# Kernel tuning notes

Measured on AMD Instinct MI355X. Metric: run time of the kernel, lower is better.

Reference implementation:

```python
import jax, jax.numpy as jnp
import numpy as np

DIM = 4096
N_HEADS = 32
N_KV_HEADS = 8
HEAD_DIM = 128
WINDOW = 1024
SEQ = 2048
ROPE_THETA = 10000.0


def setup_inputs() -> dict:
    key = jax.random.key(0)
    ks = jax.random.split(key, 5)
    x = jax.random.normal(ks[0], (SEQ, DIM), dtype=jnp.float32)
    # torch nn.Linear weights are [out_features, in_features]
    wq = jax.random.normal(ks[1], (N_HEADS * HEAD_DIM, DIM), dtype=jnp.float32) * (DIM ** -0.5)
    wk = jax.random.normal(ks[2], (N_KV_HEADS * HEAD_DIM, DIM), dtype=jnp.float32) * (DIM ** -0.5)
    wv = jax.random.normal(ks[3], (N_KV_HEADS * HEAD_DIM, DIM), dtype=jnp.float32) * (DIM ** -0.5)
    wo = jax.random.normal(ks[4], (DIM, N_HEADS * HEAD_DIM), dtype=jnp.float32) * ((N_HEADS * HEAD_DIM) ** -0.5)
    # RoPE freqs: freqs_cis[t, i] = exp(1j * t * theta^(-2i/d)); store cos/sin
    inv_freq = ROPE_THETA ** (-jnp.arange(0, HEAD_DIM, 2, dtype=jnp.float32) / HEAD_DIM)  # [D/2]
    angles = jnp.arange(SEQ, dtype=jnp.float32)[:, None] * inv_freq[None, :]  # [S, D/2]
    return {"x": x, "wq": wq, "wk": wk, "wv": wv, "wo": wo,
            "cos": jnp.cos(angles), "sin": jnp.sin(angles)}


def _apply_rope(t, cos, sin):
    # t: [S, H, D]; cos/sin: [S, D/2] -> rotate consecutive pairs as complex mul
    S, H, D = t.shape
    tr = t.reshape(S, H, D // 2, 2)
    t0, t1 = tr[..., 0], tr[..., 1]
    c = cos[:, None, :]
    s = sin[:, None, :]
    out = jnp.stack([t0 * c - t1 * s, t0 * s + t1 * c], axis=-1)
    return out.reshape(S, H, D)


def reference(x, wq, wk, wv, wo, cos, sin):
    S = x.shape[0]
    repeats = N_HEADS // N_KV_HEADS
    scale = HEAD_DIM ** -0.5
    q = (x @ wq.T).reshape(S, N_HEADS, HEAD_DIM)
    k = (x @ wk.T).reshape(S, N_KV_HEADS, HEAD_DIM)
    v = (x @ wv.T).reshape(S, N_KV_HEADS, HEAD_DIM)
    q = _apply_rope(q, cos, sin)
    k = _apply_rope(k, cos, sin)
    # repeat_kv: repeat_interleave along head axis (GQA)
    k = jnp.repeat(k, repeats, axis=1)  # [S, H, D]
    v = jnp.repeat(v, repeats, axis=1)
    scores = jnp.einsum('qhd,khd->hqk', q, k) * scale  # [H, S, S]
    # sliding-window causal mask: attend to j in (i - WINDOW, i]
    i = jnp.arange(S)[:, None]
    j = jnp.arange(S)[None, :]
    allowed = (j <= i) & (i - j < WINDOW)  # [S, S]
    scores = jnp.where(allowed[None, :, :], scores, jnp.finfo(scores.dtype).min)
    probs = jax.nn.softmax(scores, axis=-1)
    out = jnp.einsum('hqk,khd->qhd', probs, v).reshape(S, N_HEADS * HEAD_DIM)
    return out @ wo.T
```

## Files before the change

kernel.cpp:

```cpp
#include <hip/hip_runtime.h>

#define DIM 4096
#define NH 32
#define NKV 8
#define HD 128
#define WINDOW 1024
#define SEQ 2048

typedef unsigned int uint32;
typedef __attribute__((ext_vector_type(8))) short short8_t;
typedef __attribute__((ext_vector_type(8))) __bf16 bf16x8_t;
typedef __attribute__((ext_vector_type(4))) float floatx4_t;

__device__ __forceinline__ uint32 f2bf_bits(float f) {
  uint32 u = __builtin_bit_cast(uint32, f);
  return (u + 0x7fffu + ((u >> 16) & 1u)) >> 16;
}
__device__ __forceinline__ float bf2f(unsigned short b) {
  return __builtin_bit_cast(float, ((uint32)b) << 16);
}

template <class X, class Y> struct same_t { static constexpr bool v = false; };
template <class X> struct same_t<X, X> { static constexpr bool v = true; };

__device__ __forceinline__ void load_lds16(const unsigned short* g, unsigned short* l) {
  __builtin_amdgcn_global_load_lds((__attribute__((address_space(1))) void*)g,
                                   (__attribute__((address_space(3))) void*)l, 16, 0, 0);
}

template <typename TC>
__global__ __launch_bounds__(256) void gemm_bf16(const unsigned short* __restrict__ A,
                                                 const unsigned short* __restrict__ B,
                                                 TC* __restrict__ C,
                                                 int M, int N, int K) {
  __shared__ unsigned short As[128 * 64];
  __shared__ unsigned short Bs[128 * 64];
  const int tid = threadIdx.x;
  const int lane = tid & 63, w = tid >> 6;
  const int quad = lane >> 4, l16 = lane & 15;
  const int wm = w >> 1, wn = w & 1;
  const size_t m0 = (size_t)blockIdx.y * 128, n0 = (size_t)blockIdx.x * 128;

  const int srow = tid >> 3;
  const int scol = ((tid & 7) ^ (srow & 7)) << 3;
  const unsigned short* Abase = A + (m0 + srow) * (size_t)K + scol;
  const unsigned short* Bbase = B + (n0 + srow) * (size_t)K + scol;
  unsigned short* ldsA = As + (tid >> 6) * 512;
  unsigned short* ldsB = Bs + (tid >> 6) * 512;

  const int sa = l16 & 7;
  const int raA = wm * 64 + l16;
  const int raB = wn * 64 + l16;

  floatx4_t acc[4][4] = {};

  const int nk = K >> 6;
  for (int kt = 0; kt < nk; kt++) {
    const int kbase = kt << 6;
#pragma unroll
    for (int i = 0; i < 4; i++) {
      load_lds16(Abase + kbase + (size_t)(i * 32) * K, ldsA + i * 2048);
      load_lds16(Bbase + kbase + (size_t)(i * 32) * K, ldsB + i * 2048);
    }
    __syncthreads();
#pragma unroll
    for (int ks = 0; ks < 2; ks++) {
      bf16x8_t af[4], bfg[4];
#pragma unroll
      for (int i = 0; i < 4; i++) {
        const int colA = (((ks << 2) | quad) ^ sa) << 3;
        af[i] = __builtin_bit_cast(bf16x8_t,
            *(const short8_t*)(&As[(raA + i * 16) * 64 + colA]));
      }
#pragma unroll
      for (int j = 0; j < 4; j++) {
        const int colB = (((ks << 2) | quad) ^ sa) << 3;
        bfg[j] = __builtin_bit_cast(bf16x8_t,
            *(const short8_t*)(&Bs[(raB + j * 16) * 64 + colB]));
      }
#pragma unroll
      for (int i = 0; i < 4; i++)
#pragma unroll
        for (int j = 0; j < 4; j++)
          acc[i][j] = __builtin_amdgcn_mfma_f32_16x16x32_bf16(af[i], bfg[j], acc[i][j], 0, 0, 0);
    }
    __syncthreads();
  }
#pragma unroll
  for (int i = 0; i < 4; i++)
#pragma unroll
    for (int j = 0; j < 4; j++)
#pragma unroll
      for (int r = 0; r < 4; r++) {
        size_t row = m0 + wm * 64 + i * 16 + quad * 4 + r;
        size_t col = n0 + wn * 64 + j * 16 + l16;
        float v = acc[i][j][r];
        if constexpr (same_t<TC, float>::v)
          C[row * (size_t)N + col] = v;
        else
          C[row * (size_t)N + col] = (unsigned short)f2bf_bits(v);
      }
}

__global__ __launch_bounds__(256) void cvt_kernel(const float* __restrict__ in,
                                                  unsigned short* __restrict__ out, int n8) {
  int idx = blockIdx.x * 256 + threadIdx.x;
  if (idx >= n8) return;
  const float4* p = (const float4*)in + (size_t)idx * 2;
  float4 a = p[0], b = p[1];
  uint32 w0 = f2bf_bits(a.x) | (f2bf_bits(a.y) << 16);
  uint32 w1 = f2bf_bits(a.z) | (f2bf_bits(a.w) << 16);
  uint32 w2 = f2bf_bits(b.x) | (f2bf_bits(b.y) << 16);
  uint32 w3 = f2bf_bits(b.z) | (f2bf_bits(b.w) << 16);
  ((uint4*)out)[idx] = make_uint4(w0, w1, w2, w3);
}

__global__ __launch_bounds__(256) void rope_kernel(unsigned short* __restrict__ t,
                                                   const float* __restrict__ cosp,
                                                   const float* __restrict__ sinp,
                                                   int H, int ld) {
  const int idx = blockIdx.x * 256 + threadIdx.x;
  const int j = idx & 63;
  const int rem = idx >> 6;
  const int hh = rem % H;
  const int s = rem / H;
  const size_t base = (size_t)s * ld + hh * 128 + (j << 1);
  const float t0 = bf2f(t[base]), t1 = bf2f(t[base + 1]);
  const float c = cosp[s * 64 + j], sn = sinp[s * 64 + j];
  t[base] = (unsigned short)f2bf_bits(t0 * c - t1 * sn);
  t[base + 1] = (unsigned short)f2bf_bits(t0 * sn + t1 * c);
}

__global__ __launch_bounds__(256) void vtrans_kernel(const unsigned short* __restrict__ v,
                                                     unsigned short* __restrict__ vT) {
  __shared__ unsigned short t[64][72];
  const int s0 = blockIdx.y * 64, r0 = blockIdx.x * 64;
  const int tid = threadIdx.x;
#pragma unroll
  for (int it = 0; it < 2; it++) {
    int f = it * 256 + tid;
    int si = f >> 3, cj = (f & 7) << 3;
    *(short8_t*)(&t[si][cj]) = *(const short8_t*)(v + (size_t)(s0 + si) * 2048 + r0 + cj);
  }
  __syncthreads();
#pragma unroll
  for (int it = 0; it < 2; it++) {
    int f = it * 256 + tid;
    int ri = f >> 3, sj = (f & 7) << 3;
    short8_t o;
#pragma unroll
    for (int jj = 0; jj < 8; jj++) o[jj] = t[sj + jj][ri];
    *(short8_t*)(vT + (size_t)(r0 + ri) * SEQ + s0 + sj) = o;
  }
}

__global__ __launch_bounds__(256, 3) void attn_kernel(const unsigned short* __restrict__ qb,
                                                      const unsigned short* __restrict__ kb,
                                                      const unsigned short* __restrict__ vT,
                                                      unsigned short* __restrict__ attn_out) {
  const int h = blockIdx.x;
  const int qt = 31 - blockIdx.y;
  const int kvh = h >> 2;
  const int q0 = qt * 64;
  const int tid = threadIdx.x;
  const int w = tid >> 6, lane = tid & 63;
  const int quad = lane >> 4, l16 = lane & 15;
  const float SCALE = 0.08838834764831845f;

  __shared__ unsigned short Ks[64 * 128];
  __shared__ unsigned short VTs[128 * 64];
  __shared__ unsigned short PTs[4 * 64 * 34];

  unsigned short* pt = &PTs[w * 2176];

  const int krow = tid >> 4;
  const int kc16 = tid & 15;
  const int kgcol = (kc16 ^ (krow & 7)) << 3;
  const unsigned short* kgbase = kb + (size_t)krow * 2048 + kvh * 128 + kgcol;
  const int vrow = tid >> 3;
  const int vc8 = tid & 7;
  const int vgcol = (vc8 ^ (vrow & 7)) << 3;
  const unsigned short* vgbase = vT + (size_t)(kvh * 128 + vrow) * 2048 + vgcol;
  unsigned short* ldsK = Ks + w * 512;
  unsigned short* ldsV = VTs + w * 512;

  bf16x8_t aq[4];
  {
    const unsigned short* qp = qb + (size_t)(q0 + w * 16 + l16) * 4096 + h * 128 + quad * 8;
#pragma unroll
    for (int ks = 0; ks < 4; ks++)
      aq[ks] = __builtin_bit_cast(bf16x8_t, *(const short8_t*)(qp + ks * 32));
  }

  floatx4_t O[8] = {};
  float m_run[4], l_run[4];
#pragma unroll
  for (int r = 0; r < 4; r++) { m_run[r] = -3e38f; l_run[r] = 0.0f; }

  const int qmin = q0 + w * 16, qmax = qmin + 15;
  int kbeg = q0 - (WINDOW - 1); if (kbeg < 0) kbeg = 0;
  const int c0 = kbeg & ~63;
  const int nch = (q0 + 64 - c0) >> 6;
  const int sa = l16 & 7;

  for (int ci = 0; ci < nch; ci++) {
    const int kb0 = c0 + (ci << 6);
#pragma unroll
    for (int i = 0; i < 4; i++)
      load_lds16(kgbase + (size_t)(kb0 + i * 16) * 2048, ldsK + i * 2048);
#pragma unroll
    for (int i = 0; i < 4; i++)
      load_lds16(vgbase + kb0 + (size_t)(i * 32) * 2048, ldsV + i * 2048);
    __syncthreads();
    floatx4_t S[4];
#pragma unroll
    for (int j = 0; j < 4; j++) {
      floatx4_t acc = {};
      const int keyrow = j * 16 + l16;
#pragma unroll
      for (int ks = 0; ks < 4; ks++) {
        const int c16 = ((ks << 2) | quad) ^ sa;
        bf16x8_t bfk = __builtin_bit_cast(bf16x8_t,
            *(const short8_t*)(&Ks[keyrow * 128 + c16 * 8]));
        acc = __builtin_amdgcn_mfma_f32_16x16x32_bf16(aq[ks], bfk, acc, 0, 0, 0);
      }
      S[j] = acc;
    }
    const bool need_mask = (kb0 + 63 > qmin) || (qmax - kb0 >= WINDOW);
    if (need_mask) {
#pragma unroll
      for (int j = 0; j < 4; j++) {
        const int key = kb0 + j * 16 + l16;
#pragma unroll
        for (int r = 0; r < 4; r++) {
          const int i = qmin + quad * 4 + r;
          const bool ok = (key <= i) && (i - key < WINDOW);
          S[j][r] = ok ? S[j][r] : -3e38f;
        }
      }
    }
    float mx[4], rs[4], alpha[4];
#pragma unroll
    for (int r = 0; r < 4; r++) {
      float m = S[0][r];
#pragma unroll
      for (int j = 1; j < 4; j++) m = fmaxf(m, S[j][r]);
#pragma unroll
      for (int d = 1; d < 16; d <<= 1) m = fmaxf(m, __shfl_xor(m, d, 16));
      mx[r] = fmaxf(m_run[r], m);
      alpha[r] = __expf(SCALE * (m_run[r] - mx[r]));
      m_run[r] = mx[r];
      rs[r] = 0.0f;
    }
#pragma unroll
    for (int j = 0; j < 4; j++) {
      float p[4];
#pragma unroll
      for (int r = 0; r < 4; r++) {
        const float sv = S[j][r];
        float e = __expf(SCALE * (sv - mx[r]));
        if (need_mask) e = (sv < -1e37f) ? 0.0f : e;
        p[r] = e;
        rs[r] += e;
      }
      uint32* dst = (uint32*)(pt + (j * 16 + l16) * 34 + quad * 4);
      dst[0] = f2bf_bits(p[0]) | (f2bf_bits(p[1]) << 16);
      dst[1] = f2bf_bits(p[2]) | (f2bf_bits(p[3]) << 16);
    }
#pragma unroll
    for (int r = 0; r < 4; r++) {
#pragma unroll
      for (int d = 1; d < 16; d <<= 1) rs[r] += __shfl_xor(rs[r], d, 16);
      l_run[r] = l_run[r] * alpha[r] + rs[r];
    }
#pragma unroll
    for (int nt = 0; nt < 8; nt++)
#pragma unroll
      for (int r = 0; r < 4; r++) O[nt][r] *= alpha[r];
    asm volatile("" ::: "memory");
#pragma unroll
    for (int ks = 0; ks < 2; ks++) {
      short8_t as;
#pragma unroll
      for (int jj = 0; jj < 8; jj++)
        as[jj] = (short)pt[(ks * 32 + quad * 8 + jj) * 34 + l16];
      bf16x8_t af = __builtin_bit_cast(bf16x8_t, as);
#pragma unroll
      for (int nt = 0; nt < 8; nt++) {
        const int c8 = (((ks << 2) | quad) ^ sa);
        bf16x8_t bfv = __builtin_bit_cast(bf16x8_t,
            *(const short8_t*)(&VTs[(nt * 16 + l16) * 64 + c8 * 8]));
        O[nt] = __builtin_amdgcn_mfma_f32_16x16x32_bf16(af, bfv, O[nt], 0, 0, 0);
      }
    }
    __syncthreads();
  }
  float inv_l[4];
#pragma unroll
  for (int r = 0; r < 4; r++) inv_l[r] = 1.0f / l_run[r];
#pragma unroll
  for (int nt = 0; nt < 8; nt++)
#pragma unroll
    for (int r = 0; r < 4; r++) {
      float v = O[nt][r] * inv_l[r];
      attn_out[(size_t)(qmin + quad * 4 + r) * 4096 + h * 128 + nt * 16 + l16] =
          (unsigned short)f2bf_bits(v);
    }
}

extern "C" void kernel_launch(void* const* d_in, const int* in_sizes, int n_in,
                              void* d_out, int out_size, void* d_ws, size_t ws_size,
                              hipStream_t stream) {
  (void)in_sizes; (void)n_in; (void)out_size; (void)ws_size;
  const float* x    = (const float*)d_in[0];
  const float* wq   = (const float*)d_in[1];
  const float* wk   = (const float*)d_in[2];
  const float* wv   = (const float*)d_in[3];
  const float* wo   = (const float*)d_in[4];
  const float* cosp = (const float*)d_in[5];
  const float* sinp = (const float*)d_in[6];
  float* out = (float*)d_out;
  char* ws = (char*)d_ws;

  unsigned short* wqb   = (unsigned short*)(ws);
  unsigned short* attnb = (unsigned short*)(ws);
  unsigned short* vTb   = (unsigned short*)(ws + 16777216);
  unsigned short* xb    = (unsigned short*)(ws + 33554432);
  unsigned short* wkvb  = (unsigned short*)(ws + 33554432 + 16777216);
  unsigned short* wob   = (unsigned short*)(ws + 33554432);
  unsigned short* qb    = (unsigned short*)(ws + 67108864);
  unsigned short* kvb   = (unsigned short*)(ws + 83886080);

  cvt_kernel<<<4096, 256, 0, stream>>>(x, xb, SEQ * DIM / 8);
  cvt_kernel<<<8192, 256, 0, stream>>>(wq, wqb, NH * HD * DIM / 8);
  cvt_kernel<<<2048, 256, 0, stream>>>(wk, wkvb, NKV * HD * DIM / 8);
  cvt_kernel<<<2048, 256, 0, stream>>>(wv, wkvb + (size_t)NKV * HD * DIM, NKV * HD * DIM / 8);
  gemm_bf16<unsigned short><<<dim3(32, 16), 256, 0, stream>>>(xb, wqb, qb, SEQ, 4096, DIM);
  gemm_bf16<unsigned short><<<dim3(16, 16), 256, 0, stream>>>(xb, wkvb, kvb, SEQ, 2048, DIM);
  cvt_kernel<<<8192, 256, 0, stream>>>(wo, wob, DIM * NH * HD / 8);
  rope_kernel<<<SEQ * NH * 64 / 256, 256, 0, stream>>>(qb, cosp, sinp, NH, 4096);
  rope_kernel<<<SEQ * NKV * 64 / 256, 256, 0, stream>>>(kvb, cosp, sinp, NKV, 2048);
  vtrans_kernel<<<dim3(16, 32), 256, 0, stream>>>(kvb + 1024, vTb);
  attn_kernel<<<dim3(NH, 32), 256, 0, stream>>>(qb, kvb, vTb, attnb);
  gemm_bf16<float><<<dim3(32, 16), 256, 0, stream>>>(attnb, wob, out, SEQ, 4096, DIM);
}
```

Before: 530.0 us.

## Fuse QKV projection into one GEMM with RoPE epilogue and batched conversion

Concatenates the Q, K and V weights into one bf16 matrix and computes the three projections with a single GEMM of width 6144. RoPE is applied in the GEMM epilogue using a lane shuffle to fetch each pair partner, which removes both separate rope kernels and their read-modify-write passes. The four fp32-to-bf16 conversions for x, wq, wk and wv are merged into one launch, and the workspace layout and attention strides are updated for the new 6144-wide qkv buffer. The costs are cos/sin loads in the GEMM epilogue and a different workspace aliasing scheme that must stay correct.

```diff
diff --git a/kernel.cpp b/kernel.cpp
--- a/kernel.cpp
+++ b/kernel.cpp
@@ -6,6 +6,7 @@
 #define HD 128
 #define WINDOW 1024
 #define SEQ 2048
+#define QLD 6144
 
 typedef unsigned int uint32;
 typedef __attribute__((ext_vector_type(8))) short short8_t;
@@ -28,11 +29,14 @@
                                    (__attribute__((address_space(3))) void*)l, 16, 0, 0);
 }
 
-template <typename TC>
+template <typename TC, bool ROPE>
 __global__ __launch_bounds__(256) void gemm_bf16(const unsigned short* __restrict__ A,
                                                  const unsigned short* __restrict__ B,
                                                  TC* __restrict__ C,
-                                                 int M, int N, int K) {
+                                                 int M, int N, int K,
+                                                 const float* __restrict__ cosp,
+                                                 const float* __restrict__ sinp,
+                                                 int rope_ncols) {
   __shared__ unsigned short As[128 * 64];
   __shared__ unsigned short Bs[128 * 64];
   const int tid = threadIdx.x;
@@ -89,17 +93,29 @@
 #pragma unroll
   for (int i = 0; i < 4; i++)
 #pragma unroll
-    for (int j = 0; j < 4; j++)
+    for (int j = 0; j < 4; j++) {
+      const int colb = (int)n0 + wn * 64 + j * 16;
+      const bool do_rope = ROPE && (colb < rope_ncols);
 #pragma unroll
       for (int r = 0; r < 4; r++) {
         size_t row = m0 + wm * 64 + i * 16 + quad * 4 + r;
         size_t col = n0 + wn * 64 + j * 16 + l16;
         float v = acc[i][j][r];
+        if constexpr (ROPE) {
+          if (do_rope) {
+            float pv = __shfl_xor(v, 1);
+            const int d = ((int)col & 127) >> 1;
+            const float c = cosp[row * 64 + d];
+            const float s = sinp[row * 64 + d];
+            v = ((int)col & 1) ? (pv * s + v * c) : (v * c - pv * s);
+          }
+        }
         if constexpr (same_t<TC, float>::v)
           C[row * (size_t)N + col] = v;
         else
           C[row * (size_t)N + col] = (unsigned short)f2bf_bits(v);
       }
+    }
 }
 
 __global__ __launch_bounds__(256) void cvt_kernel(const float* __restrict__ in,
@@ -115,20 +131,30 @@
   ((uint4*)out)[idx] = make_uint4(w0, w1, w2, w3);
 }
 
-__global__ __launch_bounds__(256) void rope_kernel(unsigned short* __restrict__ t,
-                                                   const float* __restrict__ cosp,
-                                                   const float* __restrict__ sinp,
-                                                   int H, int ld) {
-  const int idx = blockIdx.x * 256 + threadIdx.x;
-  const int j = idx & 63;
-  const int rem = idx >> 6;
-  const int hh = rem % H;
-  const int s = rem / H;
-  const size_t base = (size_t)s * ld + hh * 128 + (j << 1);
-  const float t0 = bf2f(t[base]), t1 = bf2f(t[base + 1]);
-  const float c = cosp[s * 64 + j], sn = sinp[s * 64 + j];
-  t[base] = (unsigned short)f2bf_bits(t0 * c - t1 * sn);
-  t[base + 1] = (unsigned short)f2bf_bits(t0 * sn + t1 * c);
+__global__ __launch_bounds__(256) void cvt4_kernel(const float* __restrict__ s0,
+                                                   const float* __restrict__ s1,
+                                                   const float* __restrict__ s2,
+                                                   const float* __restrict__ s3,
+                                                   unsigned short* __restrict__ d0,
+                                                   unsigned short* __restrict__ d1,
+                                                   unsigned short* __restrict__ d2,
+                                                   unsigned short* __restrict__ d3) {
+  const int b = blockIdx.x;
+  const float* src;
+  unsigned short* dst;
+  int rb;
+  if (b < 4096)        { src = s0; dst = d0; rb = b; }
+  else if (b < 12288)  { src = s1; dst = d1; rb = b - 4096; }
+  else if (b < 14336)  { src = s2; dst = d2; rb = b - 12288; }
+  else                 { src = s3; dst = d3; rb = b - 14336; }
+  const int idx = rb * 256 + threadIdx.x;
+  const float4* p = (const float4*)src + (size_t)idx * 2;
+  float4 a = p[0], bb = p[1];
+  uint32 w0 = f2bf_bits(a.x) | (f2bf_bits(a.y) << 16);
+  uint32 w1 = f2bf_bits(a.z) | (f2bf_bits(a.w) << 16);
+  uint32 w2 = f2bf_bits(bb.x) | (f2bf_bits(bb.y) << 16);
+  uint32 w3 = f2bf_bits(bb.z) | (f2bf_bits(bb.w) << 16);
+  ((uint4*)dst)[idx] = make_uint4(w0, w1, w2, w3);
 }
 
 __global__ __launch_bounds__(256) void vtrans_kernel(const unsigned short* __restrict__ v,
@@ -140,7 +166,7 @@
   for (int it = 0; it < 2; it++) {
     int f = it * 256 + tid;
     int si = f >> 3, cj = (f & 7) << 3;
-    *(short8_t*)(&t[si][cj]) = *(const short8_t*)(v + (size_t)(s0 + si) * 2048 + r0 + cj);
+    *(short8_t*)(&t[si][cj]) = *(const short8_t*)(v + (size_t)(s0 + si) * QLD + r0 + cj);
   }
   __syncthreads();
 #pragma unroll
@@ -176,7 +202,7 @@
   const int krow = tid >> 4;
   const int kc16 = tid & 15;
   const int kgcol = (kc16 ^ (krow & 7)) << 3;
-  const unsigned short* kgbase = kb + (size_t)krow * 2048 + kvh * 128 + kgcol;
+  const unsigned short* kgbase = kb + (size_t)krow * QLD + kvh * 128 + kgcol;
   const int vrow = tid >> 3;
   const int vc8 = tid & 7;
   const int vgcol = (vc8 ^ (vrow & 7)) << 3;
@@ -186,7 +212,7 @@
 
   bf16x8_t aq[4];
   {
-    const unsigned short* qp = qb + (size_t)(q0 + w * 16 + l16) * 4096 + h * 128 + quad * 8;
+    const unsigned short* qp = qb + (size_t)(q0 + w * 16 + l16) * QLD + h * 128 + quad * 8;
 #pragma unroll
     for (int ks = 0; ks < 4; ks++)
       aq[ks] = __builtin_bit_cast(bf16x8_t, *(const short8_t*)(qp + ks * 32));
@@ -207,7 +233,7 @@
     const int kb0 = c0 + (ci << 6);
 #pragma unroll
     for (int i = 0; i < 4; i++)
-      load_lds16(kgbase + (size_t)(kb0 + i * 16) * 2048, ldsK + i * 2048);
+      load_lds16(kgbase + (size_t)(kb0 + i * 16) * QLD, ldsK + i * 2048);
 #pragma unroll
     for (int i = 0; i < 4; i++)
       load_lds16(vgbase + kb0 + (size_t)(i * 32) * 2048, ldsV + i * 2048);
@@ -322,25 +348,21 @@
   float* out = (float*)d_out;
   char* ws = (char*)d_ws;
 
-  unsigned short* wqb   = (unsigned short*)(ws);
-  unsigned short* attnb = (unsigned short*)(ws);
-  unsigned short* vTb   = (unsigned short*)(ws + 16777216);
-  unsigned short* xb    = (unsigned short*)(ws + 33554432);
-  unsigned short* wkvb  = (unsigned short*)(ws + 33554432 + 16777216);
-  unsigned short* wob   = (unsigned short*)(ws + 33554432);
-  unsigned short* qb    = (unsigned short*)(ws + 67108864);
-  unsigned short* kvb   = (unsigned short*)(ws + 83886080);
-
-  cvt_kernel<<<4096, 256, 0, stream>>>(x, xb, SEQ * DIM / 8);
-  cvt_kernel<<<8192, 256, 0, stream>>>(wq, wqb, NH * HD * DIM / 8);
-  cvt_kernel<<<2048, 256, 0, stream>>>(wk, wkvb, NKV * HD * DIM / 8);
-  cvt_kernel<<<2048, 256, 0, stream>>>(wv, wkvb + (size_t)NKV * HD * DIM, NKV * HD * DIM / 8);
-  gemm_bf16<unsigned short><<<dim3(32, 16), 256, 0, stream>>>(xb, wqb, qb, SEQ, 4096, DIM);
-  gemm_bf16<unsigned short><<<dim3(16, 16), 256, 0, stream>>>(xb, wkvb, kvb, SEQ, 2048, DIM);
+  unsigned short* wqkvb = (unsigned short*)(ws);
+  unsigned short* wob   = (unsigned short*)(ws);
+  unsigned short* vTb   = (unsigned short*)(ws + 33554432);
+  unsigned short* xb    = (unsigned short*)(ws + 50331648);
+  unsigned short* attnb = (unsigned short*)(ws + 50331648);
+  unsigned short* qkvb  = (unsigned short*)(ws + 67108864);
+
+  cvt4_kernel<<<16384, 256, 0, stream>>>(
+      x, wq, wk, wv,
+      xb, wqkvb, wqkvb + (size_t)4096 * 4096, wqkvb + (size_t)5120 * 4096);
+  gemm_bf16<unsigned short, true><<<dim3(48, 16), 256, 0, stream>>>(
+      xb, wqkvb, qkvb, SEQ, QLD, DIM, cosp, sinp, 5120);
   cvt_kernel<<<8192, 256, 0, stream>>>(wo, wob, DIM * NH * HD / 8);
-  rope_kernel<<<SEQ * NH * 64 / 256, 256, 0, stream>>>(qb, cosp, sinp, NH, 4096);
-  rope_kernel<<<SEQ * NKV * 64 / 256, 256, 0, stream>>>(kvb, cosp, sinp, NKV, 2048);
-  vtrans_kernel<<<dim3(16, 32), 256, 0, stream>>>(kvb + 1024, vTb);
-  attn_kernel<<<dim3(NH, 32), 256, 0, stream>>>(qb, kvb, vTb, attnb);
-  gemm_bf16<float><<<dim3(32, 16), 256, 0, stream>>>(attnb, wob, out, SEQ, 4096, DIM);
-}
+  vtrans_kernel<<<dim3(16, 32), 256, 0, stream>>>(qkvb + 5120, vTb);
+  attn_kernel<<<dim3(NH, 32), 256, 0, stream>>>(qkvb, qkvb + 4096, vTb, attnb);
+  gemm_bf16<float, false><<<dim3(32, 16), 256, 0, stream>>>(
+      attnb, wob, out, SEQ, 4096, DIM, nullptr, nullptr, 0);
+}
```

After: 528.2 us. About the same (-0.3%).
